# Kernel optimization log

Hardware: AMD Instinct MI355X
Metric: run time of the kernel (lower is better)

Reference implementation:

```python
import jax, jax.numpy as jnp
import numpy as np

N = 65536        # nodes
E = 131072       # directed edges
D = 512          # emb_dim
L = 5            # num_layer
G = 512          # num graphs
EPS = 1e-5       # batchnorm eps
NUM_ATOM_TYPE, NUM_CHIRALITY = 120, 3
NUM_BOND_TYPE, NUM_BOND_DIR = 6, 3


def setup_inputs() -> dict:
    key = jax.random.key(0)
    ks = jax.random.split(key, 12)
    s = 0.02
    return {
        "x": jax.random.randint(ks[0], (N, 2), 0, 3),
        "edge_index": jax.random.randint(ks[1], (2, E), 0, N),
        "edge_attr": jax.random.randint(ks[2], (E, 2), 0, 3),
        "batch": jnp.sort(jax.random.randint(ks[3], (N,), 0, G)),
        "x_emb1": jax.random.normal(ks[4], (NUM_ATOM_TYPE, D), jnp.float32) * s,
        "x_emb2": jax.random.normal(ks[5], (NUM_CHIRALITY, D), jnp.float32) * s,
        "e_emb1": jax.random.normal(ks[6], (L, NUM_BOND_TYPE, D), jnp.float32) * s,
        "e_emb2": jax.random.normal(ks[7], (L, NUM_BOND_DIR, D), jnp.float32) * s,
        "W1": jax.random.normal(ks[8], (L, D, 2 * D), jnp.float32) * s,
        "b1": jnp.zeros((L, 2 * D), jnp.float32),
        "W2": jax.random.normal(ks[9], (L, 2 * D, D), jnp.float32) * s,
        "b2": jnp.zeros((L, D), jnp.float32),
        "gamma": jnp.ones((L, D), jnp.float32),
        "beta": jnp.zeros((L, D), jnp.float32),
    }


def reference(x, edge_index, edge_attr, batch,
              x_emb1, x_emb2, e_emb1, e_emb2,
              W1, b1, W2, b2, gamma, beta):
    n = x.shape[0]
    # atom embedding: type + chirality
    h = x_emb1[x[:, 0]] + x_emb2[x[:, 1]]                     # [N, D]

    # add self loops (appended after real edges, attr = [4, 0])
    loops = jnp.arange(n)
    src = jnp.concatenate([edge_index[0], loops])             # [E+N]
    dst = jnp.concatenate([edge_index[1], loops])
    sl_attr = jnp.concatenate(
        [jnp.full((n, 1), 4, dtype=edge_attr.dtype),
         jnp.zeros((n, 1), dtype=edge_attr.dtype)], axis=1)
    ea = jnp.concatenate([edge_attr, sl_attr], axis=0)        # [E+N, 2]

    for l in range(L):
        # per-edge embedding: bond type + bond direction
        e = e_emb1[l][ea[:, 0]] + e_emb2[l][ea[:, 1]]         # [E+N, D]
        msg = h[src] + e                                      # gather + add
        agg = jax.ops.segment_sum(msg, dst, num_segments=n)   # scatter-add
        # GIN MLP: Linear(D,2D) -> ReLU -> Linear(2D,D)
        hh = jax.nn.relu(agg @ W1[l] + b1[l]) @ W2[l] + b2[l]
        # BatchNorm1d (training-mode batch statistics)
        mean = hh.mean(axis=0)
        var = hh.var(axis=0)
        hh = (hh - mean) * jax.lax.rsqrt(var + EPS) * gamma[l] + beta[l]
        if l < L - 1:
            hh = jax.nn.relu(hh)   # dropout(p=0) is identity
        h = hh

    # JK='last': node rep = h; graph rep = global mean pool over batch ids
    counts = jax.ops.segment_sum(jnp.ones((n,), h.dtype), batch, num_segments=G)
    graph = jax.ops.segment_sum(h, batch, num_segments=G) / jnp.maximum(counts, 1.0)[:, None]
    return graph, h
```

## Files before the change

### kernel.cpp

```cpp
#include <hip/hip_runtime.h>
#include <stdint.h>

#define Nn 65536
#define Ee 131072
#define Dd 512
#define D2 1024
#define Ll 5
#define Gg 512
#define EPSf 1e-5f

typedef _Float16 f16x8 __attribute__((ext_vector_type(8)));
typedef float f32x4 __attribute__((ext_vector_type(4)));
typedef unsigned short u16x8 __attribute__((ext_vector_type(8)));

__device__ __forceinline__ unsigned short f2h(float f) {
    _Float16 h = (_Float16)f;
    union { _Float16 h; unsigned short u; } c; c.h = h;
    return c.u;
}

__device__ __forceinline__ float4 h4f(ushort4 u) {
    union { unsigned short s; _Float16 h; } a, b, c, d;
    a.s = u.x; b.s = u.y; c.s = u.z; d.s = u.w;
    return make_float4((float)a.h, (float)b.h, (float)c.h, (float)d.h);
}

__device__ __forceinline__ void add4(float4& a, float4 b) {
    a.x += b.x; a.y += b.y; a.z += b.z; a.w += b.w;
}

__device__ __forceinline__ void gload_lds16(const void* g, void* l) {
    __builtin_amdgcn_global_load_lds(
        (const __attribute__((address_space(1))) void*)(uintptr_t)g,
        (__attribute__((address_space(3))) void*)(unsigned)(uintptr_t)l,
        16, 0, 0);
}

__global__ void k_transW(const float* __restrict__ src, unsigned short* __restrict__ dst,
                         int K, int Nw) {
    long total = (long)Ll * K * Nw;
    for (long idx = (long)blockIdx.x * blockDim.x + threadIdx.x; idx < total;
         idx += (long)gridDim.x * blockDim.x) {
        long l = idx / ((long)K * Nw);
        long rem = idx - l * (long)K * Nw;
        int k = (int)(rem / Nw), n = (int)(rem % Nw);
        dst[(l * Nw + n) * K + k] = f2h(src[idx]);
    }
}

__global__ void k_embed(const int* __restrict__ x,
                        const float4* __restrict__ xe1, const float4* __restrict__ xe2,
                        float4* __restrict__ h4) {
    const int total = Nn * 128;
    for (int idx = blockIdx.x * blockDim.x + threadIdx.x; idx < total;
         idx += gridDim.x * blockDim.x) {
        int node = idx >> 7, c = idx & 127;
        int t0 = x[2 * node], t1 = x[2 * node + 1];
        float4 v = xe1[t0 * 128 + c];
        float4 w = xe2[t1 * 128 + c];
        v.x += w.x; v.y += w.y; v.z += w.z; v.w += w.w;
        h4[idx] = v;
    }
}

__global__ void k_zeroN(int* __restrict__ p, int n) {
    int i = blockIdx.x * blockDim.x + threadIdx.x;
    if (i < n) p[i] = 0;
}

__global__ void k_hist(const int* __restrict__ edst, int* __restrict__ cnt) {
    int e = blockIdx.x * blockDim.x + threadIdx.x;
    if (e < Ee) atomicAdd(&cnt[edst[e]], 1);
}

__global__ void k_scan(const int* __restrict__ cnt, int* __restrict__ off,
                       int* __restrict__ cursor) {
    __shared__ int part[1024];
    int t = threadIdx.x;
    int base = t * 64;
    int s = 0;
    for (int i = 0; i < 64; ++i) s += cnt[base + i];
    part[t] = s;
    __syncthreads();
    for (int d = 1; d < 1024; d <<= 1) {
        int v = (t >= d) ? part[t - d] : 0;
        __syncthreads();
        part[t] += v;
        __syncthreads();
    }
    int run = part[t] - s;
    for (int i = 0; i < 64; ++i) {
        off[base + i] = run;
        cursor[base + i] = run;
        run += cnt[base + i];
    }
    if (t == 1023) off[Nn] = run;
}

__global__ void k_place(const int* __restrict__ esrc, const int* __restrict__ edst,
                        const int* __restrict__ eattr, int* __restrict__ cursor,
                        int* __restrict__ ckey, int* __restrict__ csrc) {
    int e = blockIdx.x * blockDim.x + threadIdx.x;
    if (e < Ee) {
        int d = edst[e];
        int p = atomicAdd(&cursor[d], 1);
        ckey[p] = e * 32 + (eattr[2 * e] * 3 + eattr[2 * e + 1]);
        csrc[p] = esrc[e];
    }
}

__global__ void k_sort(const int* __restrict__ off, int* __restrict__ ckey,
                       int* __restrict__ csrc) {
    int node = blockIdx.x * blockDim.x + threadIdx.x;
    if (node >= Nn) return;
    int kb = off[node], ke = off[node + 1];
    for (int i = kb + 1; i < ke; ++i) {
        int k = ckey[i], s = csrc[i];
        int j = i - 1;
        while (j >= kb && ckey[j] > k) {
            ckey[j + 1] = ckey[j]; csrc[j + 1] = csrc[j]; --j;
        }
        ckey[j + 1] = k; csrc[j + 1] = s;
    }
}

template <int NORM>
__global__ __launch_bounds__(256) void k_gather(const float* __restrict__ hf32,
                                                const unsigned short* __restrict__ hf16,
                                                const float* __restrict__ ss,
                                                const int* __restrict__ off,
                                                const int* __restrict__ ckey,
                                                const int* __restrict__ csrc,
                                                const float* __restrict__ e1l,
                                                const float* __restrict__ e2l,
                                                unsigned short* __restrict__ aggh) {
    int node = (blockIdx.x << 2) + (threadIdx.x >> 6);
    int lane = threadIdx.x & 63;
    int c0 = lane, c1 = lane + 64;
    float4 sa0, sb0, sa1, sb1;
    if (NORM) {
        const float4* ss4 = (const float4*)ss;
        sa0 = ss4[c0]; sb0 = ss4[128 + c0];
        sa1 = ss4[c1]; sb1 = ss4[128 + c1];
    }
    auto loadrow = [&](size_t rowbase, int c, float4 a, float4 b) -> float4 {
        float4 v;
        if (NORM) {
            v = h4f(*(const ushort4*)(hf16 + rowbase + (size_t)c * 4));
            v.x = fmaxf(fmaf(v.x, a.x, b.x), 0.f);
            v.y = fmaxf(fmaf(v.y, a.y, b.y), 0.f);
            v.z = fmaxf(fmaf(v.z, a.z, b.z), 0.f);
            v.w = fmaxf(fmaf(v.w, a.w, b.w), 0.f);
        } else {
            v = *(const float4*)(hf32 + rowbase + (size_t)c * 4);
        }
        return v;
    };
    const float4* s1 = (const float4*)(e1l + 4 * Dd);
    const float4* s2 = (const float4*)(e2l);
    size_t nb = (size_t)node * Dd;
    float4 A0 = loadrow(nb, c0, sa0, sb0);
    float4 A1 = loadrow(nb, c1, sa1, sb1);
    add4(A0, s1[c0]); add4(A0, s2[c0]);
    add4(A1, s1[c1]); add4(A1, s2[c1]);
    int kb = off[node], ke = off[node + 1];
    for (int k = kb; k < ke; ++k) {
        size_t sb = (size_t)csrc[k] * Dd;
        int at = ckey[k] & 31;
        const float4* p1 = (const float4*)(e1l + (size_t)(at / 3) * Dd);
        const float4* p2 = (const float4*)(e2l + (size_t)(at % 3) * Dd);
        add4(A0, loadrow(sb, c0, sa0, sb0)); add4(A0, p1[c0]); add4(A0, p2[c0]);
        add4(A1, loadrow(sb, c1, sa1, sb1)); add4(A1, p1[c1]); add4(A1, p2[c1]);
    }
    unsigned short* dst = aggh + (size_t)node * Dd;
    ushort4 o0, o1;
    o0.x = f2h(A0.x); o0.y = f2h(A0.y); o0.z = f2h(A0.z); o0.w = f2h(A0.w);
    o1.x = f2h(A1.x); o1.y = f2h(A1.y); o1.z = f2h(A1.z); o1.w = f2h(A1.w);
    *(ushort4*)(dst + c0 * 4) = o0;
    *(ushort4*)(dst + c1 * 4) = o1;
}

__device__ __forceinline__ void stage_q(const unsigned short* __restrict__ g, int ldk,
                                        long row0, int col0, char* region, int tid) {
    int wbase = (tid >> 6) << 10;
#pragma unroll
    for (int r = 0; r < 2; ++r) {
        int gi = tid + r * 512;
        int row = gi >> 2;
        int k16 = (gi & 3) ^ ((row >> 1) & 3);
        gload_lds16(g + (row0 + row) * (long)ldk + col0 + k16 * 8,
                    region + r * 8192 + wbase);
    }
}

__device__ __forceinline__ f16x8 rd_frag(const char* region, int row, int l4) {
    int slot = l4 ^ ((row >> 1) & 3);
    return *(const f16x8*)(region + row * 64 + (slot << 4));
}

template <int EPI>
__global__ __launch_bounds__(512, 2) void gemm8(const unsigned short* __restrict__ A,
                                                const unsigned short* __restrict__ BT,
                                                const float* __restrict__ bias,
                                                unsigned short* __restrict__ Cb,
                                                float* __restrict__ pS,
                                                int M, int N, int K) {
    __shared__ __align__(16) char lds[131072];
    const int tid = threadIdx.x;
    const int lane = tid & 63;
    const int w = tid >> 6;
    const int wm = w >> 2, wn = w & 3;
    const int l15 = lane & 15, l4 = lane >> 4;

    const int nwg = gridDim.x;
    const int cpx = nwg >> 3;
    const int bid = blockIdx.x;
    const int wg = (bid & 7) * cpx + (bid >> 3);
    const int ntn = N >> 8;
    const long bm = (long)(wg / ntn) * 256;
    const long bn = (long)(wg % ntn) * 256;

    char* Ar = lds;
    char* Br = lds + 65536;
    const int NT = K >> 6;

    f32x4 acc[8][4];
#pragma unroll
    for (int i = 0; i < 8; ++i)
#pragma unroll
        for (int j = 0; j < 4; ++j) acc[i][j] = (f32x4){0.f, 0.f, 0.f, 0.f};

    stage_q(A, K, bm, 0, Ar, tid);
    stage_q(BT, K, bn, 0, Br, tid);
    stage_q(A, K, bm, 32, Ar + 16384, tid);
    stage_q(BT, K, bn, 32, Br + 16384, tid);
    stage_q(A, K, bm, 64, Ar + 32768, tid);
    stage_q(BT, K, bn, 64, Br + 32768, tid);
    asm volatile("s_waitcnt vmcnt(8)" ::: "memory");
    __builtin_amdgcn_s_barrier();

    for (int t = 0; t < NT; ++t) {
        const int cur = (t & 1) << 1;
        const char* Ac = Ar + cur * 16384;
        const char* Bc = Br + cur * 16384;
        char* An1 = Ar + ((((t + 1) & 1) << 1) + 1) * 16384;
        char* Bn1 = Br + ((((t + 1) & 1) << 1) + 1) * 16384;
        f16x8 af[8], bv[4];

#pragma unroll
        for (int fm = 0; fm < 8; ++fm)
            af[fm] = rd_frag(Ac, wm * 128 + fm * 16 + l15, l4);
#pragma unroll
        for (int fn = 0; fn < 4; ++fn)
            bv[fn] = rd_frag(Bc, wn * 64 + fn * 16 + l15, l4);
        if (t + 1 < NT) {
            stage_q(A, K, bm, (t + 1) * 64 + 32, An1, tid);
            stage_q(BT, K, bn, (t + 1) * 64 + 32, Bn1, tid);
        }
        __builtin_amdgcn_s_barrier();
        asm volatile("s_waitcnt lgkmcnt(0)" ::: "memory");
        __builtin_amdgcn_s_setprio(1);
#pragma unroll
        for (int fm = 0; fm < 8; ++fm)
#pragma unroll
            for (int fn = 0; fn < 4; ++fn)
                acc[fm][fn] = __builtin_amdgcn_mfma_f32_16x16x32_f16(af[fm], bv[fn], acc[fm][fn], 0, 0, 0);
        __builtin_amdgcn_s_setprio(0);
        if (t >= NT - 2) {
            asm volatile("s_waitcnt vmcnt(0)" ::: "memory");
        } else {
            asm volatile("s_waitcnt vmcnt(4)" ::: "memory");
        }
        __builtin_amdgcn_s_barrier();

#pragma unroll
        for (int fm = 0; fm < 8; ++fm)
            af[fm] = rd_frag(Ac + 16384, wm * 128 + fm * 16 + l15, l4);
#pragma unroll
        for (int fn = 0; fn < 4; ++fn)
            bv[fn] = rd_frag(Bc + 16384, wn * 64 + fn * 16 + l15, l4);
        if (t + 2 < NT) {
            stage_q(A, K, bm, (t + 2) * 64, (char*)Ac, tid);
            stage_q(BT, K, bn, (t + 2) * 64, (char*)Bc, tid);
        }
        __builtin_amdgcn_s_barrier();
        asm volatile("s_waitcnt lgkmcnt(0)" ::: "memory");
        __builtin_amdgcn_s_setprio(1);
#pragma unroll
        for (int fm = 0; fm < 8; ++fm)
#pragma unroll
            for (int fn = 0; fn < 4; ++fn)
                acc[fm][fn] = __builtin_amdgcn_mfma_f32_16x16x32_f16(af[fm], bv[fn], acc[fm][fn], 0, 0, 0);
        __builtin_amdgcn_s_setprio(0);
        __builtin_amdgcn_s_barrier();
    }

    unsigned short* cl = (unsigned short*)lds;
    float cs[4] = {0.f, 0.f, 0.f, 0.f}, cq[4] = {0.f, 0.f, 0.f, 0.f};
#pragma unroll
    for (int hh = 0; hh < 2; ++hh) {
        __syncthreads();
        if (wm == hh) {
#pragma unroll
            for (int fn = 0; fn < 4; ++fn) {
                int col = wn * 64 + fn * 16 + l15;
                float bval = bias[bn + col];
#pragma unroll
                for (int fm = 0; fm < 8; ++fm) {
                    int r0 = fm * 16 + l4 * 4;
#pragma unroll
                    for (int r = 0; r < 4; ++r) {
                        float v = acc[fm][fn][r] + bval;
                        if (EPI == 0) v = fmaxf(v, 0.f);
                        else { cs[fn] += v; cq[fn] += v * v; }
                        cl[(r0 + r) * 264 + col] = f2h(v);
                    }
                }
            }
        }
        __syncthreads();
#pragma unroll
        for (int i = 0; i < 8; ++i) {
            int g = tid + i * 512;
            int r = g >> 5, cg = (g & 31) << 3;
            u16x8 val = *(const u16x8*)&cl[r * 264 + cg];
            *(u16x8*)&Cb[(bm + hh * 128 + r) * N + bn + cg] = val;
        }
    }
    if (EPI == 1) {
#pragma unroll
        for (int fn = 0; fn < 4; ++fn) {
            float s = cs[fn], q = cq[fn];
            s += __shfl_xor(s, 16); s += __shfl_xor(s, 32);
            q += __shfl_xor(q, 16); q += __shfl_xor(q, 32);
            if (l4 == 0) {
                int col = (int)bn + wn * 64 + fn * 16 + l15;
                int rowgrp = ((int)(bm >> 8)) * 2 + wm;
                pS[rowgrp * 512 + col] = s;
                pS[262144 + rowgrp * 512 + col] = q;
            }
        }
    }
}

__global__ void k_bnred(const float* __restrict__ pS, const float* __restrict__ gamma,
                        const float* __restrict__ beta, float* __restrict__ ss) {
    int col = blockIdx.x * 256 + threadIdx.x;
    float s = 0.f, q = 0.f;
    for (int rg = 0; rg < 512; ++rg) {
        s += pS[rg * 512 + col];
        q += pS[262144 + rg * 512 + col];
    }
    float mean = s * (1.f / (float)Nn);
    float var = q * (1.f / (float)Nn) - mean * mean;
    float a = gamma[col] * rsqrtf(var + EPSf);
    ss[col] = a;
    ss[512 + col] = beta[col] - mean * a;
}

__global__ void k_norm(const unsigned short* __restrict__ hhf, const float* __restrict__ ss,
                       float4* __restrict__ h4) {
    const int total = Nn * 128;
    const float4* ss4 = (const float4*)ss;
    for (int idx = blockIdx.x * blockDim.x + threadIdx.x; idx < total;
         idx += gridDim.x * blockDim.x) {
        int c = idx & 127;
        float4 v = h4f(*(const ushort4*)(hhf + (size_t)idx * 4));
        float4 a = ss4[c], b = ss4[128 + c];
        v.x = fmaf(v.x, a.x, b.x); v.y = fmaf(v.y, a.y, b.y);
        v.z = fmaf(v.z, a.z, b.z); v.w = fmaf(v.w, a.w, b.w);
        h4[idx] = v;
    }
}

__global__ void k_pool(const float* __restrict__ h, const int* __restrict__ batch,
                       float* __restrict__ graph) {
    int g = blockIdx.x, t = threadIdx.x;
    int lo = 0, hi = Nn;
    while (lo < hi) { int m = (lo + hi) >> 1; if (batch[m] < g) lo = m + 1; else hi = m; }
    int s = lo;
    lo = s; hi = Nn;
    while (lo < hi) { int m = (lo + hi) >> 1; if (batch[m] <= g) lo = m + 1; else hi = m; }
    int e = lo;
    float s0 = 0.f, s1 = 0.f;
    for (int r = s; r < e; ++r) {
        const float* row = h + (long)r * Dd;
        s0 += row[t];
        s1 += row[t + 256];
    }
    int cnt = e - s; if (cnt < 1) cnt = 1;
    float inv = 1.f / (float)cnt;
    graph[(long)g * Dd + t] = s0 * inv;
    graph[(long)g * Dd + t + 256] = s1 * inv;
}

extern "C" void kernel_launch(void* const* d_in, const int* in_sizes, int n_in,
                              void* d_out, int out_size, void* d_ws, size_t ws_size,
                              hipStream_t stream) {
    (void)in_sizes; (void)n_in; (void)out_size; (void)ws_size;
    const int* x      = (const int*)d_in[0];
    const int* ei     = (const int*)d_in[1];
    const int* ea     = (const int*)d_in[2];
    const int* batch  = (const int*)d_in[3];
    const float* xe1  = (const float*)d_in[4];
    const float* xe2  = (const float*)d_in[5];
    const float* ee1  = (const float*)d_in[6];
    const float* ee2  = (const float*)d_in[7];
    const float* W1   = (const float*)d_in[8];
    const float* b1   = (const float*)d_in[9];
    const float* W2   = (const float*)d_in[10];
    const float* b2   = (const float*)d_in[11];
    const float* gamma = (const float*)d_in[12];
    const float* beta  = (const float*)d_in[13];

    float* graph = (float*)d_out;
    float* h = graph + (size_t)Gg * Dd;

    char* w = (char*)d_ws;
    int* csr_off = (int*)w;                     w += (Nn + 1) * 4;
    int* cursor = (int*)w;                      w += Nn * 4;
    int* cnt = (int*)w;                         w += Nn * 4;
    int* ckey = (int*)w;                        w += Ee * 4;
    int* csrc = (int*)w;                        w += Ee * 4;
    float* ss = (float*)w;                      w += 4096;
    float* pS = (float*)w;                      w += 2 * 512 * 512 * 4;
    unsigned short* aggh = (unsigned short*)w;  w += (size_t)Nn * Dd * 2;
    unsigned short* hhf = (unsigned short*)w;   w += (size_t)Nn * Dd * 2;
    unsigned short* w1t = (unsigned short*)w;   w += (size_t)Ll * D2 * Dd * 2;
    unsigned short* w2t = (unsigned short*)w;   w += (size_t)Ll * Dd * D2 * 2;

    k_transW<<<2048, 256, 0, stream>>>(W1, w1t, Dd, D2);
    k_transW<<<2048, 256, 0, stream>>>(W2, w2t, D2, Dd);

    k_embed<<<2048, 256, 0, stream>>>(x, (const float4*)xe1, (const float4*)xe2, (float4*)h);

    k_zeroN<<<64, 1024, 0, stream>>>(cnt, Nn);
    k_hist<<<Ee / 256, 256, 0, stream>>>(ei + Ee, cnt);
    k_scan<<<1, 1024, 0, stream>>>(cnt, csr_off, cursor);
    k_place<<<Ee / 256, 256, 0, stream>>>(ei, ei + Ee, ea, cursor, ckey, csrc);
    k_sort<<<Nn / 256, 256, 0, stream>>>(csr_off, ckey, csrc);

    for (int l = 0; l < Ll; ++l) {
        const float* e1l = ee1 + (size_t)l * 6 * Dd;
        const float* e2l = ee2 + (size_t)l * 3 * Dd;
        if (l == 0)
            k_gather<0><<<Nn / 4, 256, 0, stream>>>(h, nullptr, nullptr, csr_off, ckey, csrc,
                                                    e1l, e2l, aggh);
        else
            k_gather<1><<<Nn / 4, 256, 0, stream>>>(nullptr, hhf, ss, csr_off, ckey, csrc,
                                                    e1l, e2l, aggh);
        gemm8<0><<<(Nn / 256) * (D2 / 256), 512, 0, stream>>>(
            aggh, w1t + (size_t)l * D2 * Dd, b1 + (size_t)l * D2,
            (unsigned short*)h, nullptr, Nn, D2, Dd);
        gemm8<1><<<(Nn / 256) * (Dd / 256), 512, 0, stream>>>(
            (const unsigned short*)h, w2t + (size_t)l * Dd * D2, b2 + (size_t)l * Dd,
            hhf, pS, Nn, Dd, D2);
        k_bnred<<<2, 256, 0, stream>>>(pS, gamma + (size_t)l * Dd, beta + (size_t)l * Dd, ss);
    }

    k_norm<<<2048, 256, 0, stream>>>(hhf, ss, (float4*)h);
    k_pool<<<Gg, 256, 0, stream>>>(h, batch, graph);
}
```

Before: 1.654 ms.

## Halve GEMM LDS to 64KB with simple double buffer, fuse BN into pooling

The GEMM kernel's shared buffer shrinks from 128KB to 64KB. Its pipeline changes from two 32-wide K stages per iteration with prefetch two ahead to a plain double buffer of one 32-wide K stage per iteration. The epilogue now writes in four 64-row passes so it fits the smaller LDS. The intent is to allow more than one workgroup per CU, which the launch bounds already request; the cost is shallower prefetch and twice as many barriers per K. Separately, the pooling kernel reads the fp16 pre-norm output and applies the BN scale/shift itself, so it no longer depends on k_norm's fp32 output.

```diff
diff --git a/kernel.cpp b/kernel.cpp
--- a/kernel.cpp
+++ b/kernel.cpp
@@ -205,7 +205,7 @@
                                                 unsigned short* __restrict__ Cb,
                                                 float* __restrict__ pS,
                                                 int M, int N, int K) {
-    __shared__ __align__(16) char lds[131072];
+    __shared__ __align__(16) char lds[65536];
     const int tid = threadIdx.x;
     const int lane = tid & 63;
     const int w = tid >> 6;
@@ -221,8 +221,8 @@
     const long bn = (long)(wg % ntn) * 256;
 
     char* Ar = lds;
-    char* Br = lds + 65536;
-    const int NT = K >> 6;
+    char* Br = lds + 32768;
+    const int NT = K >> 5;
 
     f32x4 acc[8][4];
 #pragma unroll
@@ -232,31 +232,23 @@
 
     stage_q(A, K, bm, 0, Ar, tid);
     stage_q(BT, K, bn, 0, Br, tid);
-    stage_q(A, K, bm, 32, Ar + 16384, tid);
-    stage_q(BT, K, bn, 32, Br + 16384, tid);
-    stage_q(A, K, bm, 64, Ar + 32768, tid);
-    stage_q(BT, K, bn, 64, Br + 32768, tid);
-    asm volatile("s_waitcnt vmcnt(8)" ::: "memory");
+    asm volatile("s_waitcnt vmcnt(0)" ::: "memory");
     __builtin_amdgcn_s_barrier();
 
     for (int t = 0; t < NT; ++t) {
-        const int cur = (t & 1) << 1;
-        const char* Ac = Ar + cur * 16384;
-        const char* Bc = Br + cur * 16384;
-        char* An1 = Ar + ((((t + 1) & 1) << 1) + 1) * 16384;
-        char* Bn1 = Br + ((((t + 1) & 1) << 1) + 1) * 16384;
+        const char* Ac = Ar + (t & 1) * 16384;
+        const char* Bc = Br + (t & 1) * 16384;
+        if (t + 1 < NT) {
+            stage_q(A, K, bm, (t + 1) * 32, Ar + ((t + 1) & 1) * 16384, tid);
+            stage_q(BT, K, bn, (t + 1) * 32, Br + ((t + 1) & 1) * 16384, tid);
+        }
         f16x8 af[8], bv[4];
-
 #pragma unroll
         for (int fm = 0; fm < 8; ++fm)
             af[fm] = rd_frag(Ac, wm * 128 + fm * 16 + l15, l4);
 #pragma unroll
         for (int fn = 0; fn < 4; ++fn)
             bv[fn] = rd_frag(Bc, wn * 64 + fn * 16 + l15, l4);
-        if (t + 1 < NT) {
-            stage_q(A, K, bm, (t + 1) * 64 + 32, An1, tid);
-            stage_q(BT, K, bn, (t + 1) * 64 + 32, Bn1, tid);
-        }
         __builtin_amdgcn_s_barrier();
         asm volatile("s_waitcnt lgkmcnt(0)" ::: "memory");
         __builtin_amdgcn_s_setprio(1);
@@ -266,65 +258,43 @@
             for (int fn = 0; fn < 4; ++fn)
                 acc[fm][fn] = __builtin_amdgcn_mfma_f32_16x16x32_f16(af[fm], bv[fn], acc[fm][fn], 0, 0, 0);
         __builtin_amdgcn_s_setprio(0);
-        if (t >= NT - 2) {
+        if (t + 1 < NT) {
             asm volatile("s_waitcnt vmcnt(0)" ::: "memory");
-        } else {
-            asm volatile("s_waitcnt vmcnt(4)" ::: "memory");
-        }
-        __builtin_amdgcn_s_barrier();
-
-#pragma unroll
-        for (int fm = 0; fm < 8; ++fm)
-            af[fm] = rd_frag(Ac + 16384, wm * 128 + fm * 16 + l15, l4);
-#pragma unroll
-        for (int fn = 0; fn < 4; ++fn)
-            bv[fn] = rd_frag(Bc + 16384, wn * 64 + fn * 16 + l15, l4);
-        if (t + 2 < NT) {
-            stage_q(A, K, bm, (t + 2) * 64, (char*)Ac, tid);
-            stage_q(BT, K, bn, (t + 2) * 64, (char*)Bc, tid);
-        }
-        __builtin_amdgcn_s_barrier();
-        asm volatile("s_waitcnt lgkmcnt(0)" ::: "memory");
-        __builtin_amdgcn_s_setprio(1);
-#pragma unroll
-        for (int fm = 0; fm < 8; ++fm)
-#pragma unroll
-            for (int fn = 0; fn < 4; ++fn)
-                acc[fm][fn] = __builtin_amdgcn_mfma_f32_16x16x32_f16(af[fm], bv[fn], acc[fm][fn], 0, 0, 0);
-        __builtin_amdgcn_s_setprio(0);
+        }
         __builtin_amdgcn_s_barrier();
     }
 
     unsigned short* cl = (unsigned short*)lds;
     float cs[4] = {0.f, 0.f, 0.f, 0.f}, cq[4] = {0.f, 0.f, 0.f, 0.f};
 #pragma unroll
-    for (int hh = 0; hh < 2; ++hh) {
+    for (int q = 0; q < 4; ++q) {
         __syncthreads();
-        if (wm == hh) {
+        if (wm == (q >> 1)) {
 #pragma unroll
             for (int fn = 0; fn < 4; ++fn) {
                 int col = wn * 64 + fn * 16 + l15;
                 float bval = bias[bn + col];
 #pragma unroll
-                for (int fm = 0; fm < 8; ++fm) {
-                    int r0 = fm * 16 + l4 * 4;
+                for (int fi = 0; fi < 4; ++fi) {
+                    const int fm = (q & 1) * 4 + fi;
+                    int rl = fi * 16 + l4 * 4;
 #pragma unroll
                     for (int r = 0; r < 4; ++r) {
                         float v = acc[fm][fn][r] + bval;
                         if (EPI == 0) v = fmaxf(v, 0.f);
                         else { cs[fn] += v; cq[fn] += v * v; }
-                        cl[(r0 + r) * 264 + col] = f2h(v);
+                        cl[(rl + r) * 264 + col] = f2h(v);
                     }
                 }
             }
         }
         __syncthreads();
 #pragma unroll
-        for (int i = 0; i < 8; ++i) {
+        for (int i = 0; i < 4; ++i) {
             int g = tid + i * 512;
             int r = g >> 5, cg = (g & 31) << 3;
             u16x8 val = *(const u16x8*)&cl[r * 264 + cg];
-            *(u16x8*)&Cb[(bm + hh * 128 + r) * N + bn + cg] = val;
+            *(u16x8*)&Cb[(bm + q * 64 + r) * N + bn + cg] = val;
         }
     }
     if (EPI == 1) {
@@ -373,8 +343,8 @@
     }
 }
 
-__global__ void k_pool(const float* __restrict__ h, const int* __restrict__ batch,
-                       float* __restrict__ graph) {
+__global__ void k_pool(const unsigned short* __restrict__ hhf, const float* __restrict__ ss,
+                       const int* __restrict__ batch, float* __restrict__ graph) {
     int g = blockIdx.x, t = threadIdx.x;
     int lo = 0, hi = Nn;
     while (lo < hi) { int m = (lo + hi) >> 1; if (batch[m] < g) lo = m + 1; else hi = m; }
@@ -382,11 +352,15 @@
     lo = s; hi = Nn;
     while (lo < hi) { int m = (lo + hi) >> 1; if (batch[m] <= g) lo = m + 1; else hi = m; }
     int e = lo;
+    float a0 = ss[t], a1 = ss[t + 256];
+    float b0 = ss[512 + t], b1 = ss[512 + t + 256];
+    union { unsigned short s; _Float16 h; } u0, u1;
     float s0 = 0.f, s1 = 0.f;
     for (int r = s; r < e; ++r) {
-        const float* row = h + (long)r * Dd;
-        s0 += row[t];
-        s1 += row[t + 256];
+        const unsigned short* row = hhf + (size_t)r * Dd;
+        u0.s = row[t]; u1.s = row[t + 256];
+        s0 += fmaf((float)u0.h, a0, b0);
+        s1 += fmaf((float)u1.h, a1, b1);
     }
     int cnt = e - s; if (cnt < 1) cnt = 1;
     float inv = 1.f / (float)cnt;
@@ -459,5 +433,5 @@
     }
 
     k_norm<<<2048, 256, 0, stream>>>(hhf, ss, (float4*)h);
-    k_pool<<<Gg, 256, 0, stream>>>(h, batch, graph);
-}
+    k_pool<<<Gg, 256, 0, stream>>>(hhf, ss, batch, graph);
+}
```

After: 1.678 ms. Within noise of the previous version (+1.4%).

## Restructure GEMM LDS pipeline to two-stage ping-pong with half-tile B staging

Applied to the files above, without the earlier changes.

The GEMM main loop moves from a three-slot rolling K-prefetch to a full double-buffered layout keyed on iteration parity. Each 64-wide K step is split into four MFMA phases over half of the N fragments, with A and B staging for the next step interleaved between them. This aims to spread global loads across the compute and cut register pressure (bv shrinks to 2), at the cost of more barriers per iteration. Separately, the pool kernel now reads the fp16 pre-norm buffer and applies the BN scale/shift itself, so it no longer re-reads the fp32 normalized output.

```diff
diff --git a/kernel.cpp b/kernel.cpp
--- a/kernel.cpp
+++ b/kernel.cpp
@@ -234,64 +234,91 @@
     stage_q(BT, K, bn, 0, Br, tid);
     stage_q(A, K, bm, 32, Ar + 16384, tid);
     stage_q(BT, K, bn, 32, Br + 16384, tid);
-    stage_q(A, K, bm, 64, Ar + 32768, tid);
-    stage_q(BT, K, bn, 64, Br + 32768, tid);
-    asm volatile("s_waitcnt vmcnt(8)" ::: "memory");
+    asm volatile("s_waitcnt vmcnt(4)" ::: "memory");
     __builtin_amdgcn_s_barrier();
 
     for (int t = 0; t < NT; ++t) {
-        const int cur = (t & 1) << 1;
-        const char* Ac = Ar + cur * 16384;
-        const char* Bc = Br + cur * 16384;
-        char* An1 = Ar + ((((t + 1) & 1) << 1) + 1) * 16384;
-        char* Bn1 = Br + ((((t + 1) & 1) << 1) + 1) * 16384;
-        f16x8 af[8], bv[4];
-
-#pragma unroll
-        for (int fm = 0; fm < 8; ++fm)
-            af[fm] = rd_frag(Ac, wm * 128 + fm * 16 + l15, l4);
-#pragma unroll
-        for (int fn = 0; fn < 4; ++fn)
-            bv[fn] = rd_frag(Bc, wn * 64 + fn * 16 + l15, l4);
-        if (t + 1 < NT) {
-            stage_q(A, K, bm, (t + 1) * 64 + 32, An1, tid);
-            stage_q(BT, K, bn, (t + 1) * 64 + 32, Bn1, tid);
-        }
+        const int par = (t & 1) << 15;
+        const int npar = ((t + 1) & 1) << 15;
+        const char* Ac0 = Ar + par;
+        const char* Ac1 = Ar + par + 16384;
+        const char* Bc0 = Br + par;
+        const char* Bc1 = Br + par + 16384;
+        const bool pre = (t + 1 < NT);
+        f16x8 af[8], bv[2];
+
+#pragma unroll
+        for (int fm = 0; fm < 8; ++fm)
+            af[fm] = rd_frag(Ac0, wm * 128 + fm * 16 + l15, l4);
+#pragma unroll
+        for (int fn = 0; fn < 2; ++fn)
+            bv[fn] = rd_frag(Bc0, wn * 64 + fn * 16 + l15, l4);
+        if (pre) stage_q(BT, K, bn, (t + 1) * 64, Br + npar, tid);
         __builtin_amdgcn_s_barrier();
         asm volatile("s_waitcnt lgkmcnt(0)" ::: "memory");
         __builtin_amdgcn_s_setprio(1);
 #pragma unroll
         for (int fm = 0; fm < 8; ++fm)
 #pragma unroll
-            for (int fn = 0; fn < 4; ++fn)
+            for (int fn = 0; fn < 2; ++fn)
                 acc[fm][fn] = __builtin_amdgcn_mfma_f32_16x16x32_f16(af[fm], bv[fn], acc[fm][fn], 0, 0, 0);
         __builtin_amdgcn_s_setprio(0);
-        if (t >= NT - 2) {
-            asm volatile("s_waitcnt vmcnt(0)" ::: "memory");
-        } else {
-            asm volatile("s_waitcnt vmcnt(4)" ::: "memory");
-        }
-        __builtin_amdgcn_s_barrier();
-
-#pragma unroll
-        for (int fm = 0; fm < 8; ++fm)
-            af[fm] = rd_frag(Ac + 16384, wm * 128 + fm * 16 + l15, l4);
-#pragma unroll
-        for (int fn = 0; fn < 4; ++fn)
-            bv[fn] = rd_frag(Bc + 16384, wn * 64 + fn * 16 + l15, l4);
-        if (t + 2 < NT) {
-            stage_q(A, K, bm, (t + 2) * 64, (char*)Ac, tid);
-            stage_q(BT, K, bn, (t + 2) * 64, (char*)Bc, tid);
-        }
+        __builtin_amdgcn_s_barrier();
+
+#pragma unroll
+        for (int fn = 0; fn < 2; ++fn)
+            bv[fn] = rd_frag(Bc0, wn * 64 + 32 + fn * 16 + l15, l4);
+        if (pre) stage_q(A, K, bm, (t + 1) * 64, Ar + npar, tid);
         __builtin_amdgcn_s_barrier();
         asm volatile("s_waitcnt lgkmcnt(0)" ::: "memory");
         __builtin_amdgcn_s_setprio(1);
 #pragma unroll
         for (int fm = 0; fm < 8; ++fm)
 #pragma unroll
-            for (int fn = 0; fn < 4; ++fn)
+            for (int fn = 0; fn < 2; ++fn)
+                acc[fm][2 + fn] = __builtin_amdgcn_mfma_f32_16x16x32_f16(af[fm], bv[fn], acc[fm][2 + fn], 0, 0, 0);
+        __builtin_amdgcn_s_setprio(0);
+        if (pre) {
+            asm volatile("s_waitcnt vmcnt(4)" ::: "memory");
+        } else {
+            asm volatile("s_waitcnt vmcnt(0)" ::: "memory");
+        }
+        __builtin_amdgcn_s_barrier();
+
+#pragma unroll
+        for (int fm = 0; fm < 8; ++fm)
+            af[fm] = rd_frag(Ac1, wm * 128 + fm * 16 + l15, l4);
+#pragma unroll
+        for (int fn = 0; fn < 2; ++fn)
+            bv[fn] = rd_frag(Bc1, wn * 64 + fn * 16 + l15, l4);
+        if (pre) stage_q(BT, K, bn, (t + 1) * 64 + 32, Br + npar + 16384, tid);
+        __builtin_amdgcn_s_barrier();
+        asm volatile("s_waitcnt lgkmcnt(0)" ::: "memory");
+        __builtin_amdgcn_s_setprio(1);
+#pragma unroll
+        for (int fm = 0; fm < 8; ++fm)
+#pragma unroll
+            for (int fn = 0; fn < 2; ++fn)
                 acc[fm][fn] = __builtin_amdgcn_mfma_f32_16x16x32_f16(af[fm], bv[fn], acc[fm][fn], 0, 0, 0);
         __builtin_amdgcn_s_setprio(0);
+        __builtin_amdgcn_s_barrier();
+
+#pragma unroll
+        for (int fn = 0; fn < 2; ++fn)
+            bv[fn] = rd_frag(Bc1, wn * 64 + 32 + fn * 16 + l15, l4);
+        if (pre) stage_q(A, K, bm, (t + 1) * 64 + 32, Ar + npar + 16384, tid);
+        __builtin_amdgcn_s_barrier();
+        asm volatile("s_waitcnt lgkmcnt(0)" ::: "memory");
+        __builtin_amdgcn_s_setprio(1);
+#pragma unroll
+        for (int fm = 0; fm < 8; ++fm)
+#pragma unroll
+            for (int fn = 0; fn < 2; ++fn)
+                acc[fm][2 + fn] = __builtin_amdgcn_mfma_f32_16x16x32_f16(af[fm], bv[fn], acc[fm][2 + fn], 0, 0, 0);
+        __builtin_amdgcn_s_setprio(0);
+        if (pre) {
+            asm volatile("s_waitcnt vmcnt(4)" ::: "memory");
+        }
         __builtin_amdgcn_s_barrier();
     }
 
@@ -373,8 +400,8 @@
     }
 }
 
-__global__ void k_pool(const float* __restrict__ h, const int* __restrict__ batch,
-                       float* __restrict__ graph) {
+__global__ void k_pool(const unsigned short* __restrict__ hhf, const float* __restrict__ ss,
+                       const int* __restrict__ batch, float* __restrict__ graph) {
     int g = blockIdx.x, t = threadIdx.x;
     int lo = 0, hi = Nn;
     while (lo < hi) { int m = (lo + hi) >> 1; if (batch[m] < g) lo = m + 1; else hi = m; }
@@ -382,11 +409,15 @@
     lo = s; hi = Nn;
     while (lo < hi) { int m = (lo + hi) >> 1; if (batch[m] <= g) lo = m + 1; else hi = m; }
     int e = lo;
+    float a0 = ss[t], a1 = ss[t + 256];
+    float b0 = ss[512 + t], b1 = ss[512 + t + 256];
+    union { unsigned short s; _Float16 h; } u0, u1;
     float s0 = 0.f, s1 = 0.f;
     for (int r = s; r < e; ++r) {
-        const float* row = h + (long)r * Dd;
-        s0 += row[t];
-        s1 += row[t + 256];
+        const unsigned short* row = hhf + (size_t)r * Dd;
+        u0.s = row[t]; u1.s = row[t + 256];
+        s0 += fmaf((float)u0.h, a0, b0);
+        s1 += fmaf((float)u1.h, a1, b1);
     }
     int cnt = e - s; if (cnt < 1) cnt = 1;
     float inv = 1.f / (float)cnt;
@@ -459,5 +490,5 @@
     }
 
     k_norm<<<2048, 256, 0, stream>>>(hhf, ss, (float4*)h);
-    k_pool<<<Gg, 256, 0, stream>>>(h, batch, graph);
-}
+    k_pool<<<Gg, 256, 0, stream>>>(hhf, ss, batch, graph);
+}
```

Result: faster. 1.620 ms (-2.1%).
